# Performance work log

Hardware: AMD Instinct MI355X
Metric: run time of the kernel (lower is better)

Reference implementation:

```python
import jax, jax.numpy as jnp
import numpy as np

N_U = 100000   # num 'u' nodes
N_V = 100000   # num 'v' nodes (destination type)
D = 128        # feature dim
E1 = 3200000   # edges ('u','r1','v')
E2 = 3200000   # edges ('v','r2','v')


def setup_inputs() -> dict:
    key = jax.random.key(0)
    ks = jax.random.split(key, 10)
    inv = 1.0 / np.sqrt(D)
    inv3 = 1.0 / np.sqrt(3 * D)
    return {
        "x_u": jax.random.normal(ks[0], (N_U, D), jnp.float32),
        "x_v": jax.random.normal(ks[1], (N_V, D), jnp.float32),
        "W_r1": jax.random.normal(ks[2], (D, D), jnp.float32) * inv,
        "W_r2": jax.random.normal(ks[3], (D, D), jnp.float32) * inv,
        "W_gate": jax.random.normal(ks[4], (3 * D, 3 * D), jnp.float32) * inv3,
        "b_gate": jnp.zeros((3 * D,), jnp.float32),
        "W_aggr": jax.random.normal(ks[5], (3 * D, D), jnp.float32) * inv3,
        "b_aggr": jnp.zeros((D,), jnp.float32),
        "edge_index_r1": jax.random.randint(ks[6], (2, E1), 0, N_V, dtype=jnp.int64),
        "edge_index_r2": jax.random.randint(ks[7], (2, E2), 0, N_V, dtype=jnp.int64),
    }


def reference(x_u, x_v, W_r1, W_r2, W_gate, b_gate, W_aggr, b_aggr,
              edge_index_r1, edge_index_r2):
    n_v = x_v.shape[0]
    # per-edge-type conv: gather source features, per-relation linear message
    msg1 = x_u[edge_index_r1[0]] @ W_r1   # [E1, D]
    msg2 = x_v[edge_index_r2[0]] @ W_r2   # [E2, D]
    # concat all relations targeting dst 'v' (as in out_dict concatenation)
    msg = jnp.concatenate([msg1, msg2], axis=0)              # [E1+E2, D]
    idx = jnp.concatenate([edge_index_r1[1], edge_index_r2[1]])  # [E1+E2]
    # sum aggregation (scatter_add into zeros of shape [N_v, D])
    s = jax.ops.segment_sum(msg, idx, num_segments=n_v)
    # mean = sum / count.clamp(min=1)
    cnt = jax.ops.segment_sum(jnp.ones_like(msg), idx, num_segments=n_v)
    mean = s / jnp.clip(cnt, 1.0)
    # max with include_self=True over zero-initialized output -> max(msgs, 0), empty rows = 0
    mx = jnp.maximum(jax.ops.segment_max(msg, idx, num_segments=n_v), 0.0)
    total = jnp.concatenate([s, mean, mx], axis=1)           # [N_v, 3D]
    mask = jnp.sum(jnp.abs(total), axis=1) == 0              # untouched nodes
    gate = jax.nn.sigmoid(total @ W_gate + b_gate)           # attention gate
    out = (total * gate) @ W_aggr + b_aggr                   # [N_v, D]
    return jnp.where(mask[:, None], 0.0, out)
```

## Files before the change

kernel.cpp:

```cpp
#include <hip/hip_runtime.h>
#include <math.h>

#define N_U 100000
#define N_V 100000
#define D 128
#define E1 3200000
#define E2 3200000
#define ETOT (E1 + E2)

#define NBUCK 196
#define SLACK 35000
#define PCHUNK 4096
#define CSTRIDE 32

#define NBL_V 1563
#define NBL_U 1563
#define NBL_P 1563

typedef __bf16 bf16x8 __attribute__((ext_vector_type(8)));
typedef float f32x4 __attribute__((ext_vector_type(4)));

__device__ __forceinline__ unsigned short f2b(float f) {
  union { float f; unsigned int u; } v; v.f = f;
  unsigned int u = v.u;
  unsigned int r = u + 0x7fffu + ((u >> 16) & 1u);
  return (unsigned short)(r >> 16);
}
__device__ __forceinline__ float b2f(unsigned short s) {
  union { unsigned int u; float f; } v; v.u = ((unsigned int)s) << 16; return v.f;
}
__device__ __forceinline__ float b2f_lo(unsigned w) {
  union { unsigned u; float f; } v; v.u = w << 16; return v.f;
}
__device__ __forceinline__ float b2f_hi(unsigned w) {
  union { unsigned u; float f; } v; v.u = w & 0xffff0000u; return v.f;
}

__global__ __launch_bounds__(256) void convert_all(
    const float* __restrict__ W_r1, const float* __restrict__ W_r2,
    const float* __restrict__ W_gate, const float* __restrict__ W_aggr,
    unsigned short* __restrict__ Wr1F, unsigned short* __restrict__ Wr2F,
    unsigned short* __restrict__ WgF, unsigned short* __restrict__ WaF) {
  const int b = blockIdx.x;
  if (b < 128) {
    const float* W = (b < 64) ? W_r1 : W_r2;
    unsigned short* WF = (b < 64) ? Wr1F : Wr2F;
    int idx = (b & 63) * 256 + threadIdx.x;
    int k = idx >> 7, n = idx & 127;
    int f = (n >> 4) * 4 + (k >> 5);
    int out = f * 512 + ((n & 15) + 16 * ((k >> 3) & 3)) * 8 + (k & 7);
    WF[out] = f2b(W[k * 128 + n]);
  } else if (b < 704) {
    int idx = (b - 128) * 256 + threadIdx.x;
    int k = idx / 384, n = idx - k * 384;
    int f = (n >> 4) * 12 + (k >> 5);
    int out = f * 512 + ((n & 15) + 16 * ((k >> 3) & 3)) * 8 + (k & 7);
    WgF[out] = f2b(W_gate[k * 384 + n]);
  } else {
    int idx = (b - 704) * 256 + threadIdx.x;
    int k = idx >> 7, n = idx & 127;
    int f = (n >> 4) * 12 + (k >> 5);
    int out = f * 512 + ((n & 15) + 16 * ((k >> 3) & 3)) * 8 + (k & 7);
    WaF[out] = f2b(W_aggr[k * 128 + n]);
  }
}

#define LM 64
union SMem1 {
  struct { unsigned short Xs[LM][136]; } lin;
  struct {
    int hist[256]; int scan_s[256]; int lstart[256];
    int gbase[NBUCK]; int lcur[NBUCK];
    uint2 buf[PCHUNK];
  } part;
};

__device__ __forceinline__ void do_linear(
    const float* __restrict__ X, const unsigned short* __restrict__ WF,
    unsigned short* __restrict__ Hb, int nrows, int bid, SMem1& sm) {
  const int t = threadIdx.x;
  const int row0 = bid * LM;

  for (int i = t * 4; i < LM * 128; i += 1024) {
    int n = i >> 7, j = i & 127;
    int r = row0 + n;
    float4 v = make_float4(0.f, 0.f, 0.f, 0.f);
    if (r < nrows) v = *(const float4*)&X[(size_t)r * 128 + j];
    unsigned long long w =
        (unsigned long long)f2b(v.x) |
        ((unsigned long long)f2b(v.y) << 16) |
        ((unsigned long long)f2b(v.z) << 32) |
        ((unsigned long long)f2b(v.w) << 48);
    *(unsigned long long*)&sm.lin.Xs[n][j] = w;
  }
  __syncthreads();

  const int wv = t >> 6;
  const int ln = t & 63;
  const int lr = ln & 15;
  const int lq = ln >> 4;
  const int m0 = wv * 16;

  bf16x8 a[4];
#pragma unroll
  for (int ks = 0; ks < 4; ks++)
    a[ks] = *(const bf16x8*)&sm.lin.Xs[m0 + lr][ks * 32 + lq * 8];
  __syncthreads();

#pragma unroll
  for (int np = 0; np < 4; np++) {
    const int n0 = np * 32;
    f32x4 acc0 = {0.f, 0.f, 0.f, 0.f};
    f32x4 acc1 = {0.f, 0.f, 0.f, 0.f};
    const unsigned short* B0 = WF + (size_t)(np * 2) * 4 * 512 + ln * 8;
    const unsigned short* B1 = B0 + 4 * 512;
#pragma unroll
    for (int ks = 0; ks < 4; ks++) {
      bf16x8 b0 = *(const bf16x8*)(B0 + ks * 512);
      bf16x8 b1 = *(const bf16x8*)(B1 + ks * 512);
      acc0 = __builtin_amdgcn_mfma_f32_16x16x32_bf16(a[ks], b0, acc0, 0, 0, 0);
      acc1 = __builtin_amdgcn_mfma_f32_16x16x32_bf16(a[ks], b1, acc1, 0, 0, 0);
    }
#pragma unroll
    for (int r = 0; r < 4; r++) {
      int row = m0 + lq * 4 + r;
      sm.lin.Xs[row][n0 + lr] = f2b(acc0[r]);
      sm.lin.Xs[row][n0 + 16 + lr] = f2b(acc1[r]);
    }
  }
  __syncthreads();

  {
    int row = t >> 2, part = t & 3;
    int grow = row0 + row;
    if (grow < nrows) {
      uint4* dst = (uint4*)&Hb[(size_t)grow * 128 + part * 32];
      const unsigned short* src = &sm.lin.Xs[row][part * 32];
      uint4 w0 = *(const uint4*)(src);
      uint4 w1 = *(const uint4*)(src + 8);
      uint4 w2 = *(const uint4*)(src + 16);
      uint4 w3 = *(const uint4*)(src + 24);
      dst[0] = w0; dst[1] = w1; dst[2] = w2; dst[3] = w3;
    }
  }
}

__device__ __forceinline__ void do_partition(
    const int* __restrict__ e1, const int* __restrict__ e2,
    int* __restrict__ bucketCursor, unsigned* __restrict__ recs,
    int bid, SMem1& sm) {
  const int t = threadIdx.x;
  const long base = (long)bid * PCHUNK;
  const int n = (int)min((long)PCHUNK, (long)ETOT - base);

  sm.part.hist[t] = 0;
  __syncthreads();

  uint2 myrec[PCHUNK / 256];
  int myb[PCHUNK / 256];
#pragma unroll
  for (int k = 0; k < PCHUNK / 256; k++) {
    int idx = t + k * 256;
    int enc = 0, dst = 0;
    if (idx < n) {
      long i = base + idx;
      if (i < E1) {
        dst = e1[E1 + i];
        enc = N_V + e1[i];
      } else {
        long j = i - E1;
        dst = e2[E2 + j];
        enc = e2[j];
      }
      atomicAdd(&sm.part.hist[dst >> 9], 1);
    }
    myrec[k] = make_uint2(((unsigned)enc << 9) | ((unsigned)dst & 511u),
                          (unsigned)(dst >> 9));
    myb[k] = dst >> 9;
  }
  __syncthreads();

  int v = sm.part.hist[t];
  sm.part.scan_s[t] = v;
  __syncthreads();
  for (int off = 1; off < 256; off <<= 1) {
    int tmp = (t >= off) ? sm.part.scan_s[t - off] : 0;
    __syncthreads();
    sm.part.scan_s[t] += tmp;
    __syncthreads();
  }
  sm.part.lstart[t] = sm.part.scan_s[t] - v;
  if (t < NBUCK) {
    sm.part.gbase[t] = atomicAdd(&bucketCursor[t * CSTRIDE], v);
    sm.part.lcur[t] = sm.part.scan_s[t] - v;
  }
  __syncthreads();

#pragma unroll
  for (int k = 0; k < PCHUNK / 256; k++) {
    int idx = t + k * 256;
    if (idx < n) {
      int p = atomicAdd(&sm.part.lcur[myb[k]], 1);
      sm.part.buf[p] = myrec[k];
    }
  }
  __syncthreads();

  for (int p = t; p < n; p += 256) {
    uint2 r = sm.part.buf[p];
    int b = (int)r.y;
    recs[(size_t)b * SLACK + sm.part.gbase[b] + (p - sm.part.lstart[b])] = r.x;
  }
}

__global__ __launch_bounds__(256) void stage1(
    const float* __restrict__ x_v, const float* __restrict__ x_u,
    const unsigned short* __restrict__ Wr2F, const unsigned short* __restrict__ Wr1F,
    unsigned short* __restrict__ Hb,
    const int* __restrict__ e1, const int* __restrict__ e2,
    int* __restrict__ bucketCursor, unsigned* __restrict__ recs) {
  __shared__ SMem1 sm;
  const int b = blockIdx.x;
  if (b < NBL_P) {
    do_partition(e1, e2, bucketCursor, recs, b, sm);
  } else if (b < NBL_P + NBL_V) {
    do_linear(x_v, Wr2F, Hb, N_V, b - NBL_P, sm);
  } else {
    do_linear(x_u, Wr1F, Hb + (size_t)N_V * D, N_U, b - NBL_P - NBL_V, sm);
  }
}

__global__ __launch_bounds__(1024) void bucket_fill(
    const unsigned* __restrict__ recs, const int* __restrict__ bucketCnt,
    int* __restrict__ row_ptr, int* __restrict__ col) {
  __shared__ int hist[512];
  __shared__ int s[512];
  __shared__ int curF[512];
  __shared__ int curB[512];
  __shared__ int sh_outBase;
  const int t = threadIdx.x;
  const int b = blockIdx.x;
  const size_t slack = (size_t)b * SLACK;
  const int n = bucketCnt[b * CSTRIDE];
  const int n0 = b << 9;
  (void)n0;

  int cv = 0;
  if (t < 256) {
    cv = (t < NBUCK) ? bucketCnt[t * CSTRIDE] : 0;
    s[t] = cv;
  }
  __syncthreads();
  for (int off = 1; off < 256; off <<= 1) {
    int tmp = 0;
    if (t < 256 && t >= off) tmp = s[t - off];
    __syncthreads();
    if (t < 256) s[t] += tmp;
    __syncthreads();
  }
  if (t == b) sh_outBase = s[t] - cv;
  __syncthreads();
  const int outBase = sh_outBase;

  if (t < 512) hist[t] = 0;
  __syncthreads();
  for (int p = t; p < n; p += 1024)
    atomicAdd(&hist[recs[slack + p] & 511u], 1);
  __syncthreads();

  int v = 0;
  if (t < 512) {
    v = hist[t];
    s[t] = v;
  }
  __syncthreads();
  for (int off = 1; off < 512; off <<= 1) {
    int tmp = 0;
    if (t < 512 && t >= off) tmp = s[t - off];
    __syncthreads();
    if (t < 512) s[t] += tmp;
    __syncthreads();
  }
  if (t < 512) {
    int excl = s[t] - v;
    curF[t] = excl;
    curB[t] = excl + v;
    int nd = (b << 9) + t;
    if (nd < N_V) row_ptr[nd] = outBase + excl;
  }
  if (b == 0 && t == 0) row_ptr[N_V] = ETOT;
  __syncthreads();

  for (int p = t; p < n; p += 1024) {
    unsigned r = recs[slack + p];
    int local = (int)(r & 511u);
    unsigned enc = r >> 9;
    int q;
    if (enc >= (unsigned)N_V) q = atomicSub(&curB[local], 1) - 1;
    else q = atomicAdd(&curF[local], 1);
    col[outBase + q] = (int)(enc << 8);
  }
}

#define AGG1(w)                                        \
  do {                                                 \
    float lo = b2f_lo(w), hi = b2f_hi(w);              \
    s[2 * q] += lo; s[2 * q + 1] += hi;                \
    m[2 * q] = fmaxf(m[2 * q], lo);                    \
    m[2 * q + 1] = fmaxf(m[2 * q + 1], hi);            \
  } while (0)

__global__ __launch_bounds__(256) void aggregate_kernel(
    const unsigned short* __restrict__ Hb, const int* __restrict__ row_ptr,
    const int* __restrict__ col, unsigned int* __restrict__ SumB,
    unsigned int* __restrict__ MxB, int nodeBase) {
  const int node = nodeBase + blockIdx.x * 4 + (threadIdx.x >> 6);
  const int lane = threadIdx.x & 63;
  const int grp = lane >> 4;
  const int fl = lane & 15;
  const int start = row_ptr[node];
  const int end = row_ptr[node + 1];
  const char* Hc = (const char*)Hb;
  const int byteoff = fl * 16;

  float s[8] = {0.f, 0.f, 0.f, 0.f, 0.f, 0.f, 0.f, 0.f};
  float m[8] = {0.f, 0.f, 0.f, 0.f, 0.f, 0.f, 0.f, 0.f};

  int i = start;
  for (; i + 31 < end; i += 32) {
    uint4 v[8];
#pragma unroll
    for (int g = 0; g < 8; g++) {
      int e = i + g * 4 + grp;
      v[g] = *(const uint4*)(Hc + (unsigned)col[e] + byteoff);
    }
#pragma unroll
    for (int g = 0; g < 8; g++) {
      { int q = 0; AGG1(v[g].x); }
      { int q = 1; AGG1(v[g].y); }
      { int q = 2; AGG1(v[g].z); }
      { int q = 3; AGG1(v[g].w); }
    }
  }
  for (; i < end; i += 4) {
    int e = i + grp;
    int ec = e < end ? e : (end - 1);
    uint4 v = *(const uint4*)(Hc + (unsigned)col[ec] + byteoff);
    if (e >= end) { v.x = 0u; v.y = 0u; v.z = 0u; v.w = 0u; }
    { int q = 0; AGG1(v.x); }
    { int q = 1; AGG1(v.y); }
    { int q = 2; AGG1(v.z); }
    { int q = 3; AGG1(v.w); }
  }

#pragma unroll
  for (int k = 0; k < 8; k++) {
    s[k] += __shfl_xor(s[k], 16, 64);
    m[k] = fmaxf(m[k], __shfl_xor(m[k], 16, 64));
    s[k] += __shfl_xor(s[k], 32, 64);
    m[k] = fmaxf(m[k], __shfl_xor(m[k], 32, 64));
  }

  if (lane < 16) {
    uint4 o;
    o.x = (unsigned)f2b(s[0]) | ((unsigned)f2b(s[1]) << 16);
    o.y = (unsigned)f2b(s[2]) | ((unsigned)f2b(s[3]) << 16);
    o.z = (unsigned)f2b(s[4]) | ((unsigned)f2b(s[5]) << 16);
    o.w = (unsigned)f2b(s[6]) | ((unsigned)f2b(s[7]) << 16);
    ((uint4*)SumB)[(size_t)node * 16 + fl] = o;
  } else if (lane < 32) {
    uint4 o;
    o.x = (unsigned)f2b(m[0]) | ((unsigned)f2b(m[1]) << 16);
    o.y = (unsigned)f2b(m[2]) | ((unsigned)f2b(m[3]) << 16);
    o.z = (unsigned)f2b(m[4]) | ((unsigned)f2b(m[5]) << 16);
    o.w = (unsigned)f2b(m[6]) | ((unsigned)f2b(m[7]) << 16);
    ((uint4*)MxB)[(size_t)node * 16 + fl] = o;
  }
}

#define EM 64
__global__ __launch_bounds__(256, 3) void epilogue_mfma(
    const unsigned short* __restrict__ SumB, const unsigned short* __restrict__ MxB,
    const int* __restrict__ row_ptr, const unsigned short* __restrict__ WgF,
    const float* __restrict__ bg, const unsigned short* __restrict__ WaF,
    const float* __restrict__ ba, float* __restrict__ Out) {
  __shared__ unsigned short Ts[EM][392];
  __shared__ float invs[EM];
  __shared__ int cnts[EM];

  const int t = threadIdx.x;
  const int node0 = blockIdx.x * EM;

  if (t < EM) {
    int nd = node0 + t;
    int c = 0;
    if (nd < N_V) c = row_ptr[nd + 1] - row_ptr[nd];
    cnts[t] = c;
    invs[t] = 1.0f / (float)(c > 0 ? c : 1);
  }
  __syncthreads();

  {
    const uint4* Sv = (const uint4*)SumB;
    const uint4* Mv = (const uint4*)MxB;
    for (int i = t; i < EM * 16; i += 256) {
      int n = i >> 4, u = i & 15;
      int nd = node0 + n;
      uint4 s = make_uint4(0u, 0u, 0u, 0u);
      uint4 m4 = make_uint4(0u, 0u, 0u, 0u);
      if (nd < N_V) {
        s = Sv[(size_t)nd * 16 + u];
        m4 = Mv[(size_t)nd * 16 + u];
      }
      float inv = invs[n];
      *(uint4*)&Ts[n][u * 8] = s;
      unsigned sw[4] = {s.x, s.y, s.z, s.w};
      unsigned mr[4];
#pragma unroll
      for (int q = 0; q < 4; q++) {
        unsigned short lo = f2b(b2f((unsigned short)sw[q]) * inv);
        unsigned short hi = f2b(b2f((unsigned short)(sw[q] >> 16)) * inv);
        mr[q] = (unsigned)lo | ((unsigned)hi << 16);
      }
      *(uint4*)&Ts[n][128 + u * 8] = make_uint4(mr[0], mr[1], mr[2], mr[3]);
      *(uint4*)&Ts[n][256 + u * 8] = m4;
    }
  }
  __syncthreads();

  const int wv = t >> 6;
  const int ln = t & 63;
  const int lr = ln & 15;
  const int lq = ln >> 4;

  f32x4 acc[4][6];
#pragma unroll
  for (int m = 0; m < 4; m++)
#pragma unroll
    for (int nt = 0; nt < 6; nt++) acc[m][nt] = (f32x4){0.f, 0.f, 0.f, 0.f};

  const unsigned short* Bg = WgF + (size_t)(wv * 6) * 12 * 512 + ln * 8;

#pragma unroll 2
  for (int kc = 0; kc < 12; kc++) {
    bf16x8 b[6];
#pragma unroll
    for (int nt = 0; nt < 6; nt++)
      b[nt] = *(const bf16x8*)(Bg + (nt * 12 + kc) * 512);
    bf16x8 a[4];
#pragma unroll
    for (int m = 0; m < 4; m++)
      a[m] = *(const bf16x8*)&Ts[m * 16 + lr][kc * 32 + lq * 8];
#pragma unroll
    for (int m = 0; m < 4; m++)
#pragma unroll
      for (int nt = 0; nt < 6; nt++)
        acc[m][nt] = __builtin_amdgcn_mfma_f32_16x16x32_bf16(a[m], b[nt], acc[m][nt], 0, 0, 0);
  }
  __syncthreads();

#pragma unroll
  for (int nt = 0; nt < 6; nt++) {
    int cg = wv * 96 + nt * 16 + lr;
    float bgv = bg[cg];
#pragma unroll
    for (int m = 0; m < 4; m++) {
#pragma unroll
      for (int r = 0; r < 4; r++) {
        int row = m * 16 + lq * 4 + r;
        float g = 1.f / (1.f + __expf(-(acc[m][nt][r] + bgv)));
        Ts[row][cg] = f2b(b2f(Ts[row][cg]) * g);
      }
    }
  }
  __syncthreads();

  f32x4 acc2[4][2];
#pragma unroll
  for (int m = 0; m < 4; m++)
#pragma unroll
    for (int nt = 0; nt < 2; nt++) acc2[m][nt] = (f32x4){0.f, 0.f, 0.f, 0.f};

  const unsigned short* Ba = WaF + (size_t)(wv * 2) * 12 * 512 + ln * 8;

#pragma unroll 2
  for (int kc = 0; kc < 12; kc++) {
    bf16x8 b[2];
#pragma unroll
    for (int nt = 0; nt < 2; nt++)
      b[nt] = *(const bf16x8*)(Ba + (nt * 12 + kc) * 512);
    bf16x8 a[4];
#pragma unroll
    for (int m = 0; m < 4; m++)
      a[m] = *(const bf16x8*)&Ts[m * 16 + lr][kc * 32 + lq * 8];
#pragma unroll
    for (int m = 0; m < 4; m++)
#pragma unroll
      for (int nt = 0; nt < 2; nt++)
        acc2[m][nt] = __builtin_amdgcn_mfma_f32_16x16x32_bf16(a[m], b[nt], acc2[m][nt], 0, 0, 0);
  }

#pragma unroll
  for (int nt = 0; nt < 2; nt++) {
    int cg = wv * 32 + nt * 16 + lr;
    float bav = ba[cg];
#pragma unroll
    for (int m = 0; m < 4; m++) {
#pragma unroll
      for (int r = 0; r < 4; r++) {
        int row = m * 16 + lq * 4 + r;
        int nd = node0 + row;
        if (nd < N_V) {
          float msk = (cnts[row] > 0) ? 1.f : 0.f;
          Out[(size_t)nd * D + cg] = (acc2[m][nt][r] + bav) * msk;
        }
      }
    }
  }
}

extern "C" void kernel_launch(void* const* d_in, const int* in_sizes, int n_in,
                              void* d_out, int out_size, void* d_ws, size_t ws_size,
                              hipStream_t stream) {
  const float* x_u = (const float*)d_in[0];
  const float* x_v = (const float*)d_in[1];
  const float* W_r1 = (const float*)d_in[2];
  const float* W_r2 = (const float*)d_in[3];
  const float* W_gate = (const float*)d_in[4];
  const float* b_gate = (const float*)d_in[5];
  const float* W_aggr = (const float*)d_in[6];
  const float* b_aggr = (const float*)d_in[7];
  const int* e1 = (const int*)d_in[8];
  const int* e2 = (const int*)d_in[9];
  float* out = (float*)d_out;

  char* ws = (char*)d_ws;
  size_t off = 0;
  unsigned short* Hb = (unsigned short*)(ws + off); off += (size_t)(N_V + N_U) * D * 2;
  unsigned int* SumB = (unsigned int*)(ws + off);   off += (size_t)N_V * D * 2;
  unsigned int* MxB = (unsigned int*)(ws + off);    off += (size_t)N_V * D * 2;
  int* colA = (int*)(ws + off);        off += (size_t)ETOT * 4;
  unsigned* recs = (unsigned*)(ws + off); off += (size_t)NBUCK * SLACK * 4;
  int* row_ptr = (int*)(ws + off);     off += (size_t)(N_V + 1) * 4;
  int* bucketCursor = (int*)(ws + off); off += (size_t)NBUCK * CSTRIDE * 4;
  unsigned short* Wg16 = (unsigned short*)(ws + off); off += (size_t)384 * 384 * 2;
  unsigned short* Wa16 = (unsigned short*)(ws + off); off += (size_t)128 * 384 * 2;
  unsigned short* Wr1T = (unsigned short*)(ws + off); off += (size_t)128 * 128 * 2;
  unsigned short* Wr2T = (unsigned short*)(ws + off); off += (size_t)128 * 128 * 2;

  hipMemsetAsync(bucketCursor, 0, (size_t)NBUCK * CSTRIDE * 4, stream);

  convert_all<<<896, 256, 0, stream>>>(W_r1, W_r2, W_gate, W_aggr,
                                       Wr1T, Wr2T, Wg16, Wa16);

  stage1<<<NBL_P + NBL_V + NBL_U, 256, 0, stream>>>(
      x_v, x_u, Wr2T, Wr1T, Hb, e1, e2, bucketCursor, recs);

  bucket_fill<<<NBUCK, 1024, 0, stream>>>(recs, bucketCursor, row_ptr, colA);

  aggregate_kernel<<<N_V / 8, 256, 0, stream>>>(Hb, row_ptr, colA, SumB, MxB, 0);
  aggregate_kernel<<<N_V / 8, 256, 0, stream>>>(Hb, row_ptr, colA, SumB, MxB, N_V / 2);

  epilogue_mfma<<<(N_V + EM - 1) / EM, 256, 0, stream>>>(
      (const unsigned short*)SumB, (const unsigned short*)MxB, row_ptr,
      Wg16, b_gate, Wa16, b_aggr, out);
}
```

Measured before the change: 577.4 us.

## Fuse neighbor aggregation into MFMA gated epilogue kernel

```diff
diff --git a/kernel.cpp b/kernel.cpp
--- a/kernel.cpp
+++ b/kernel.cpp
@@ -242,8 +242,6 @@
   const int b = blockIdx.x;
   const size_t slack = (size_t)b * SLACK;
   const int n = bucketCnt[b * CSTRIDE];
-  const int n0 = b << 9;
-  (void)n0;
 
   int cv = 0;
   if (t < 256) {
@@ -310,78 +308,10 @@
     m[2 * q + 1] = fmaxf(m[2 * q + 1], hi);            \
   } while (0)
 
-__global__ __launch_bounds__(256) void aggregate_kernel(
+#define EM 64
+__global__ __launch_bounds__(256, 3) void agg_epilogue(
     const unsigned short* __restrict__ Hb, const int* __restrict__ row_ptr,
-    const int* __restrict__ col, unsigned int* __restrict__ SumB,
-    unsigned int* __restrict__ MxB, int nodeBase) {
-  const int node = nodeBase + blockIdx.x * 4 + (threadIdx.x >> 6);
-  const int lane = threadIdx.x & 63;
-  const int grp = lane >> 4;
-  const int fl = lane & 15;
-  const int start = row_ptr[node];
-  const int end = row_ptr[node + 1];
-  const char* Hc = (const char*)Hb;
-  const int byteoff = fl * 16;
-
-  float s[8] = {0.f, 0.f, 0.f, 0.f, 0.f, 0.f, 0.f, 0.f};
-  float m[8] = {0.f, 0.f, 0.f, 0.f, 0.f, 0.f, 0.f, 0.f};
-
-  int i = start;
-  for (; i + 31 < end; i += 32) {
-    uint4 v[8];
-#pragma unroll
-    for (int g = 0; g < 8; g++) {
-      int e = i + g * 4 + grp;
-      v[g] = *(const uint4*)(Hc + (unsigned)col[e] + byteoff);
-    }
-#pragma unroll
-    for (int g = 0; g < 8; g++) {
-      { int q = 0; AGG1(v[g].x); }
-      { int q = 1; AGG1(v[g].y); }
-      { int q = 2; AGG1(v[g].z); }
-      { int q = 3; AGG1(v[g].w); }
-    }
-  }
-  for (; i < end; i += 4) {
-    int e = i + grp;
-    int ec = e < end ? e : (end - 1);
-    uint4 v = *(const uint4*)(Hc + (unsigned)col[ec] + byteoff);
-    if (e >= end) { v.x = 0u; v.y = 0u; v.z = 0u; v.w = 0u; }
-    { int q = 0; AGG1(v.x); }
-    { int q = 1; AGG1(v.y); }
-    { int q = 2; AGG1(v.z); }
-    { int q = 3; AGG1(v.w); }
-  }
-
-#pragma unroll
-  for (int k = 0; k < 8; k++) {
-    s[k] += __shfl_xor(s[k], 16, 64);
-    m[k] = fmaxf(m[k], __shfl_xor(m[k], 16, 64));
-    s[k] += __shfl_xor(s[k], 32, 64);
-    m[k] = fmaxf(m[k], __shfl_xor(m[k], 32, 64));
-  }
-
-  if (lane < 16) {
-    uint4 o;
-    o.x = (unsigned)f2b(s[0]) | ((unsigned)f2b(s[1]) << 16);
-    o.y = (unsigned)f2b(s[2]) | ((unsigned)f2b(s[3]) << 16);
-    o.z = (unsigned)f2b(s[4]) | ((unsigned)f2b(s[5]) << 16);
-    o.w = (unsigned)f2b(s[6]) | ((unsigned)f2b(s[7]) << 16);
-    ((uint4*)SumB)[(size_t)node * 16 + fl] = o;
-  } else if (lane < 32) {
-    uint4 o;
-    o.x = (unsigned)f2b(m[0]) | ((unsigned)f2b(m[1]) << 16);
-    o.y = (unsigned)f2b(m[2]) | ((unsigned)f2b(m[3]) << 16);
-    o.z = (unsigned)f2b(m[4]) | ((unsigned)f2b(m[5]) << 16);
-    o.w = (unsigned)f2b(m[6]) | ((unsigned)f2b(m[7]) << 16);
-    ((uint4*)MxB)[(size_t)node * 16 + fl] = o;
-  }
-}
-
-#define EM 64
-__global__ __launch_bounds__(256, 3) void epilogue_mfma(
-    const unsigned short* __restrict__ SumB, const unsigned short* __restrict__ MxB,
-    const int* __restrict__ row_ptr, const unsigned short* __restrict__ WgF,
+    const int* __restrict__ col, const unsigned short* __restrict__ WgF,
     const float* __restrict__ bg, const unsigned short* __restrict__ WaF,
     const float* __restrict__ ba, float* __restrict__ Out) {
   __shared__ unsigned short Ts[EM][392];
@@ -400,44 +330,95 @@
   }
   __syncthreads();
 
-  {
-    const uint4* Sv = (const uint4*)SumB;
-    const uint4* Mv = (const uint4*)MxB;
-    for (int i = t; i < EM * 16; i += 256) {
-      int n = i >> 4, u = i & 15;
-      int nd = node0 + n;
-      uint4 s = make_uint4(0u, 0u, 0u, 0u);
-      uint4 m4 = make_uint4(0u, 0u, 0u, 0u);
-      if (nd < N_V) {
-        s = Sv[(size_t)nd * 16 + u];
-        m4 = Mv[(size_t)nd * 16 + u];
+  const int wv = t >> 6;
+  const int lane = t & 63;
+  const int grp = lane >> 4;
+  const int fl = lane & 15;
+  const char* Hc = (const char*)Hb;
+  const int byteoff = fl * 16;
+
+  for (int i = 0; i < 16; i++) {
+    const int n = (wv << 4) + i;
+    const int node = node0 + n;
+    int start = 0, end = 0;
+    if (node < N_V) { start = row_ptr[node]; end = row_ptr[node + 1]; }
+
+    float s[8] = {0.f, 0.f, 0.f, 0.f, 0.f, 0.f, 0.f, 0.f};
+    float m[8] = {0.f, 0.f, 0.f, 0.f, 0.f, 0.f, 0.f, 0.f};
+
+    int e0 = start;
+    for (; e0 + 31 < end; e0 += 32) {
+      uint4 v[8];
+#pragma unroll
+      for (int g = 0; g < 8; g++) {
+        int e = e0 + g * 4 + grp;
+        v[g] = *(const uint4*)(Hc + (unsigned)col[e] + byteoff);
       }
+#pragma unroll
+      for (int g = 0; g < 8; g++) {
+        { int q = 0; AGG1(v[g].x); }
+        { int q = 1; AGG1(v[g].y); }
+        { int q = 2; AGG1(v[g].z); }
+        { int q = 3; AGG1(v[g].w); }
+      }
+    }
+    for (; e0 < end; e0 += 4) {
+      int e = e0 + grp;
+      int ec = e < end ? e : (end - 1);
+      uint4 v = *(const uint4*)(Hc + (unsigned)col[ec] + byteoff);
+      if (e >= end) { v.x = 0u; v.y = 0u; v.z = 0u; v.w = 0u; }
+      { int q = 0; AGG1(v.x); }
+      { int q = 1; AGG1(v.y); }
+      { int q = 2; AGG1(v.z); }
+      { int q = 3; AGG1(v.w); }
+    }
+
+#pragma unroll
+    for (int k = 0; k < 8; k++) {
+      s[k] += __shfl_xor(s[k], 16, 64);
+      m[k] = fmaxf(m[k], __shfl_xor(m[k], 16, 64));
+      s[k] += __shfl_xor(s[k], 32, 64);
+      m[k] = fmaxf(m[k], __shfl_xor(m[k], 32, 64));
+    }
+
+    if (lane < 16) {
+      uint4 o;
+      o.x = (unsigned)f2b(s[0]) | ((unsigned)f2b(s[1]) << 16);
+      o.y = (unsigned)f2b(s[2]) | ((unsigned)f2b(s[3]) << 16);
+      o.z = (unsigned)f2b(s[4]) | ((unsigned)f2b(s[5]) << 16);
+      o.w = (unsigned)f2b(s[6]) | ((unsigned)f2b(s[7]) << 16);
+      *(uint4*)&Ts[n][fl * 8] = o;
       float inv = invs[n];
-      *(uint4*)&Ts[n][u * 8] = s;
-      unsigned sw[4] = {s.x, s.y, s.z, s.w};
-      unsigned mr[4];
-#pragma unroll
-      for (int q = 0; q < 4; q++) {
-        unsigned short lo = f2b(b2f((unsigned short)sw[q]) * inv);
-        unsigned short hi = f2b(b2f((unsigned short)(sw[q] >> 16)) * inv);
-        mr[q] = (unsigned)lo | ((unsigned)hi << 16);
-      }
-      *(uint4*)&Ts[n][128 + u * 8] = make_uint4(mr[0], mr[1], mr[2], mr[3]);
-      *(uint4*)&Ts[n][256 + u * 8] = m4;
-    }
-  }
-  __syncthreads();
-
-  const int wv = t >> 6;
-  const int ln = t & 63;
+      uint4 om;
+      om.x = (unsigned)f2b(b2f((unsigned short)o.x) * inv) |
+             ((unsigned)f2b(b2f((unsigned short)(o.x >> 16)) * inv) << 16);
+      om.y = (unsigned)f2b(b2f((unsigned short)o.y) * inv) |
+             ((unsigned)f2b(b2f((unsigned short)(o.y >> 16)) * inv) << 16);
+      om.z = (unsigned)f2b(b2f((unsigned short)o.z) * inv) |
+             ((unsigned)f2b(b2f((unsigned short)(o.z >> 16)) * inv) << 16);
+      om.w = (unsigned)f2b(b2f((unsigned short)o.w) * inv) |
+             ((unsigned)f2b(b2f((unsigned short)(o.w >> 16)) * inv) << 16);
+      *(uint4*)&Ts[n][128 + fl * 8] = om;
+    } else if (lane < 32) {
+      uint4 o;
+      o.x = (unsigned)f2b(m[0]) | ((unsigned)f2b(m[1]) << 16);
+      o.y = (unsigned)f2b(m[2]) | ((unsigned)f2b(m[3]) << 16);
+      o.z = (unsigned)f2b(m[4]) | ((unsigned)f2b(m[5]) << 16);
+      o.w = (unsigned)f2b(m[6]) | ((unsigned)f2b(m[7]) << 16);
+      *(uint4*)&Ts[n][256 + fl * 8] = o;
+    }
+  }
+  __syncthreads();
+
+  const int ln = lane;
   const int lr = ln & 15;
   const int lq = ln >> 4;
 
   f32x4 acc[4][6];
 #pragma unroll
-  for (int m = 0; m < 4; m++)
-#pragma unroll
-    for (int nt = 0; nt < 6; nt++) acc[m][nt] = (f32x4){0.f, 0.f, 0.f, 0.f};
+  for (int m2 = 0; m2 < 4; m2++)
+#pragma unroll
+    for (int nt = 0; nt < 6; nt++) acc[m2][nt] = (f32x4){0.f, 0.f, 0.f, 0.f};
 
   const unsigned short* Bg = WgF + (size_t)(wv * 6) * 12 * 512 + ln * 8;
 
@@ -449,13 +430,13 @@
       b[nt] = *(const bf16x8*)(Bg + (nt * 12 + kc) * 512);
     bf16x8 a[4];
 #pragma unroll
-    for (int m = 0; m < 4; m++)
-      a[m] = *(const bf16x8*)&Ts[m * 16 + lr][kc * 32 + lq * 8];
-#pragma unroll
-    for (int m = 0; m < 4; m++)
+    for (int m2 = 0; m2 < 4; m2++)
+      a[m2] = *(const bf16x8*)&Ts[m2 * 16 + lr][kc * 32 + lq * 8];
+#pragma unroll
+    for (int m2 = 0; m2 < 4; m2++)
 #pragma unroll
       for (int nt = 0; nt < 6; nt++)
-        acc[m][nt] = __builtin_amdgcn_mfma_f32_16x16x32_bf16(a[m], b[nt], acc[m][nt], 0, 0, 0);
+        acc[m2][nt] = __builtin_amdgcn_mfma_f32_16x16x32_bf16(a[m2], b[nt], acc[m2][nt], 0, 0, 0);
   }
   __syncthreads();
 
@@ -464,11 +445,11 @@
     int cg = wv * 96 + nt * 16 + lr;
     float bgv = bg[cg];
 #pragma unroll
-    for (int m = 0; m < 4; m++) {
+    for (int m2 = 0; m2 < 4; m2++) {
 #pragma unroll
       for (int r = 0; r < 4; r++) {
-        int row = m * 16 + lq * 4 + r;
-        float g = 1.f / (1.f + __expf(-(acc[m][nt][r] + bgv)));
+        int row = m2 * 16 + lq * 4 + r;
+        float g = 1.f / (1.f + __expf(-(acc[m2][nt][r] + bgv)));
         Ts[row][cg] = f2b(b2f(Ts[row][cg]) * g);
       }
     }
@@ -477,9 +458,9 @@
 
   f32x4 acc2[4][2];
 #pragma unroll
-  for (int m = 0; m < 4; m++)
-#pragma unroll
-    for (int nt = 0; nt < 2; nt++) acc2[m][nt] = (f32x4){0.f, 0.f, 0.f, 0.f};
+  for (int m2 = 0; m2 < 4; m2++)
+#pragma unroll
+    for (int nt = 0; nt < 2; nt++) acc2[m2][nt] = (f32x4){0.f, 0.f, 0.f, 0.f};
 
   const unsigned short* Ba = WaF + (size_t)(wv * 2) * 12 * 512 + ln * 8;
 
@@ -491,13 +472,13 @@
       b[nt] = *(const bf16x8*)(Ba + (nt * 12 + kc) * 512);
     bf16x8 a[4];
 #pragma unroll
-    for (int m = 0; m < 4; m++)
-      a[m] = *(const bf16x8*)&Ts[m * 16 + lr][kc * 32 + lq * 8];
-#pragma unroll
-    for (int m = 0; m < 4; m++)
+    for (int m2 = 0; m2 < 4; m2++)
+      a[m2] = *(const bf16x8*)&Ts[m2 * 16 + lr][kc * 32 + lq * 8];
+#pragma unroll
+    for (int m2 = 0; m2 < 4; m2++)
 #pragma unroll
       for (int nt = 0; nt < 2; nt++)
-        acc2[m][nt] = __builtin_amdgcn_mfma_f32_16x16x32_bf16(a[m], b[nt], acc2[m][nt], 0, 0, 0);
+        acc2[m2][nt] = __builtin_amdgcn_mfma_f32_16x16x32_bf16(a[m2], b[nt], acc2[m2][nt], 0, 0, 0);
   }
 
 #pragma unroll
@@ -505,14 +486,14 @@
     int cg = wv * 32 + nt * 16 + lr;
     float bav = ba[cg];
 #pragma unroll
-    for (int m = 0; m < 4; m++) {
+    for (int m2 = 0; m2 < 4; m2++) {
 #pragma unroll
       for (int r = 0; r < 4; r++) {
-        int row = m * 16 + lq * 4 + r;
+        int row = m2 * 16 + lq * 4 + r;
         int nd = node0 + row;
         if (nd < N_V) {
           float msk = (cnts[row] > 0) ? 1.f : 0.f;
-          Out[(size_t)nd * D + cg] = (acc2[m][nt][r] + bav) * msk;
+          Out[(size_t)nd * D + cg] = (acc2[m2][nt][r] + bav) * msk;
         }
       }
     }
@@ -537,8 +518,6 @@
   char* ws = (char*)d_ws;
   size_t off = 0;
   unsigned short* Hb = (unsigned short*)(ws + off); off += (size_t)(N_V + N_U) * D * 2;
-  unsigned int* SumB = (unsigned int*)(ws + off);   off += (size_t)N_V * D * 2;
-  unsigned int* MxB = (unsigned int*)(ws + off);    off += (size_t)N_V * D * 2;
   int* colA = (int*)(ws + off);        off += (size_t)ETOT * 4;
   unsigned* recs = (unsigned*)(ws + off); off += (size_t)NBUCK * SLACK * 4;
   int* row_ptr = (int*)(ws + off);     off += (size_t)(N_V + 1) * 4;
@@ -558,10 +537,6 @@
 
   bucket_fill<<<NBUCK, 1024, 0, stream>>>(recs, bucketCursor, row_ptr, colA);
 
-  aggregate_kernel<<<N_V / 8, 256, 0, stream>>>(Hb, row_ptr, colA, SumB, MxB, 0);
-  aggregate_kernel<<<N_V / 8, 256, 0, stream>>>(Hb, row_ptr, colA, SumB, MxB, N_V / 2);
-
-  epilogue_mfma<<<(N_V + EM - 1) / EM, 256, 0, stream>>>(
-      (const unsigned short*)SumB, (const unsigned short*)MxB, row_ptr,
-      Wg16, b_gate, Wa16, b_aggr, out);
-}
+  agg_epilogue<<<(N_V + EM - 1) / EM, 256, 0, stream>>>(
+      Hb, row_ptr, colA, Wg16, b_gate, Wa16, b_aggr, out);
+}
```

After: 713.4 us. 23.5% more time.
